# Kernel optimization log

Measured on AMD Instinct MI355X. Metric: run time of the kernel, lower is better.

## Reference

```python
import jax, jax.numpy as jnp
import numpy as np

NUM_EMBEDDINGS = 1024
EMBEDDING_DIM = 64


def setup_inputs() -> dict:
    key = jax.random.key(0)
    kx, kw = jax.random.split(key)
    x = jax.random.normal(kx, (8, 128, 128, EMBEDDING_DIM), dtype=jnp.float32)
    W = jax.random.normal(kw, (NUM_EMBEDDINGS, EMBEDDING_DIM), dtype=jnp.float32)
    return {"x": x, "W": W}


def reference(x, W):
    # Flatten to [N, D]
    flat = x.reshape(-1, EMBEDDING_DIM)
    # ||f||^2 + ||w||^2 - 2 f.w  -> [N, K]
    f_sq = jnp.sum(flat * flat, axis=1, keepdims=True)          # [N, 1]
    w_sq = jnp.sum(W * W, axis=1)                               # [K]
    prod = 2.0 * jnp.einsum('nd,kd->nk', flat, W)               # [N, K]
    distances = f_sq + w_sq - prod
    indices = jnp.argmin(distances, axis=1)                     # [N]
    # one_hot @ W is an exact gather of codebook rows
    quantized = W[indices].reshape(x.shape)
    quantized_with_grad = x + jax.lax.stop_gradient(quantized - x)
    return (quantized_with_grad, quantized, indices)
```

## Files before the change

kernel.cpp:

```cpp
#include <hip/hip_runtime.h>

#define VQ_D 64
#define VQ_MARGIN 0.015f

typedef __attribute__((ext_vector_type(8))) short bf16x8;
typedef __attribute__((ext_vector_type(4))) float f32x4;

static __device__ __forceinline__ unsigned short bf16_rne(float v) {
    unsigned u = __float_as_uint(v);
    u += 0x7fffu + ((u >> 16) & 1u);
    return (unsigned short)(u >> 16);
}

__global__ __launch_bounds__(256) void vq_prep_kernel(
    const float* __restrict__ W, unsigned short* __restrict__ Whi,
    unsigned short* __restrict__ Wlo, float* __restrict__ wsq,
    unsigned int* __restrict__ ctr, int K)
{
    int c = blockIdx.x * 256 + threadIdx.x;
    if (c == 0) *ctr = 0u;
    if (c >= K) return;
    const float4* wr = reinterpret_cast<const float4*>(W) + (size_t)c * (VQ_D / 4);
    unsigned short* hr = Whi + (size_t)c * VQ_D;
    unsigned short* lr = Wlo + (size_t)c * VQ_D;
    float s0 = 0.f, s1 = 0.f, s2 = 0.f, s3 = 0.f;
    #pragma unroll
    for (int j = 0; j < VQ_D / 4; ++j) {
        float4 v = wr[j];
        s0 = __fmaf_rn(v.x, v.x, s0); s1 = __fmaf_rn(v.y, v.y, s1);
        s2 = __fmaf_rn(v.z, v.z, s2); s3 = __fmaf_rn(v.w, v.w, s3);
        float vv[4] = {v.x, v.y, v.z, v.w};
        ushort4 h4, l4;
        unsigned short* hp = &h4.x; unsigned short* lp = &l4.x;
        #pragma unroll
        for (int e = 0; e < 4; ++e) {
            unsigned short hb = bf16_rne(vv[e]);
            float hf = __uint_as_float((unsigned)hb << 16);
            hp[e] = hb;
            lp[e] = bf16_rne(vv[e] - hf);
        }
        *reinterpret_cast<ushort4*>(hr + 4 * j) = h4;
        *reinterpret_cast<ushort4*>(lr + 4 * j) = l4;
    }
    wsq[c] = (s0 + s1) + (s2 + s3);
}

__global__ __launch_bounds__(256) void vq_mfma_kernel(
    const float* __restrict__ x, const unsigned short* __restrict__ Whi,
    const unsigned short* __restrict__ Wlo, const float* __restrict__ wsq,
    int* __restrict__ idx_final, int* __restrict__ flags,
    unsigned int* __restrict__ ctr, int N, int K)
{
    __shared__ float sD1[4][64], sD2[4][64];
    __shared__ int   sI1[4][64];

    const int tid  = threadIdx.x;
    const int wv   = tid >> 6;
    const int lane = tid & 63;
    const int g    = lane >> 4;
    const int c16  = lane & 15;
    const int rbase = blockIdx.x * 64;

    bf16x8 xh[4][2], xl[4][2];
    #pragma unroll
    for (int s = 0; s < 4; ++s) {
        int row = rbase + s * 16 + c16;
        if (row >= N) row = N - 1;
        const float* xr = x + (size_t)row * VQ_D;
        #pragma unroll
        for (int h = 0; h < 2; ++h) {
            const float4* p = reinterpret_cast<const float4*>(xr + h * 32 + g * 8);
            float4 v0 = p[0], v1 = p[1];
            float vv[8] = {v0.x, v0.y, v0.z, v0.w, v1.x, v1.y, v1.z, v1.w};
            #pragma unroll
            for (int j = 0; j < 8; ++j) {
                unsigned short hb = bf16_rne(vv[j]);
                float hf = __uint_as_float((unsigned)hb << 16);
                xh[s][h][j] = (short)hb;
                xl[s][h][j] = (short)bf16_rne(vv[j] - hf);
            }
        }
    }

    float d1[4][4], d2[4][4]; int i1[4][4];
    #pragma unroll
    for (int s = 0; s < 4; ++s)
        #pragma unroll
        for (int i = 0; i < 4; ++i) { d1[s][i] = 3.4e38f; d2[s][i] = 3.4e38f; i1[s][i] = 0; }

    const int t0 = wv * (K >> 6);
    const int t1 = t0 + (K >> 6);
    #pragma unroll 2
    for (int ct = t0; ct < t1; ++ct) {
        const int c = ct * 16 + c16;
        const unsigned short* wh = Whi + (size_t)c * VQ_D + g * 8;
        const unsigned short* wl = Wlo + (size_t)c * VQ_D + g * 8;
        bf16x8 bh0 = *reinterpret_cast<const bf16x8*>(wh);
        bf16x8 bh1 = *reinterpret_cast<const bf16x8*>(wh + 32);
        bf16x8 bl0 = *reinterpret_cast<const bf16x8*>(wl);
        bf16x8 bl1 = *reinterpret_cast<const bf16x8*>(wl + 32);
        const float wq = wsq[c];

        #pragma unroll
        for (int s = 0; s < 4; ++s) {
            f32x4 acc = {0.f, 0.f, 0.f, 0.f};
            acc = __builtin_amdgcn_mfma_f32_16x16x32_bf16(xh[s][0], bh0, acc, 0, 0, 0);
            acc = __builtin_amdgcn_mfma_f32_16x16x32_bf16(xh[s][1], bh1, acc, 0, 0, 0);
            acc = __builtin_amdgcn_mfma_f32_16x16x32_bf16(xl[s][0], bh0, acc, 0, 0, 0);
            acc = __builtin_amdgcn_mfma_f32_16x16x32_bf16(xl[s][1], bh1, acc, 0, 0, 0);
            acc = __builtin_amdgcn_mfma_f32_16x16x32_bf16(xh[s][0], bl0, acc, 0, 0, 0);
            acc = __builtin_amdgcn_mfma_f32_16x16x32_bf16(xh[s][1], bl1, acc, 0, 0, 0);
            #pragma unroll
            for (int i = 0; i < 4; ++i) {
                float d = __fmaf_rn(-2.0f, acc[i], wq);
                float o1 = d1[s][i];
                d2[s][i] = fminf(d2[s][i], fmaxf(d, o1));
                bool lt = d < o1;
                d1[s][i] = lt ? d : o1;
                i1[s][i] = lt ? c : i1[s][i];
            }
        }
    }

    #pragma unroll
    for (int s = 0; s < 4; ++s)
        #pragma unroll
        for (int i = 0; i < 4; ++i) {
            float a1 = d1[s][i], a2 = d2[s][i]; int ai = i1[s][i];
            #pragma unroll
            for (int m = 1; m < 16; m <<= 1) {
                float o1 = __shfl_xor(a1, m, 64);
                float o2 = __shfl_xor(a2, m, 64);
                int   oi = __shfl_xor(ai, m, 64);
                float n1 = fminf(a1, o1);
                a2 = fminf(fminf(a2, o2), fmaxf(a1, o1));
                ai = (o1 < a1) ? oi : ai;
                a1 = n1;
            }
            if (c16 == 0) {
                int r = s * 16 + g * 4 + i;
                sD1[wv][r] = a1; sD2[wv][r] = a2; sI1[wv][r] = ai;
            }
        }
    __syncthreads();

    if (tid < 64) {
        int row = rbase + tid;
        float m1 = sD1[0][tid], m2 = sD2[0][tid]; int mi = sI1[0][tid];
        #pragma unroll
        for (int w = 1; w < 4; ++w) {
            float a = sD1[w][tid], b = sD2[w][tid]; int ii = sI1[w][tid];
            if (a < m1) { m2 = fminf(m1, b); mi = ii; m1 = a; }
            else        { m2 = fminf(m2, a); }
        }
        if (row < N) {
            idx_final[row] = mi;
            if (m2 - m1 <= VQ_MARGIN) {
                unsigned int pos = atomicAdd(ctr, 1u);
                if (pos < (unsigned)N) flags[pos] = row;
            }
        }
    }
}

__global__ __launch_bounds__(256) void vq_recheck_kernel(
    const float* __restrict__ x, const float* __restrict__ W,
    const float* __restrict__ wsq, const int* __restrict__ flags,
    const unsigned int* __restrict__ ctr, int* __restrict__ idx_final, int N, int K)
{
    __shared__ float sBD[4];
    __shared__ int   sBI[4];

    const int tid  = threadIdx.x;
    const int wv   = tid >> 6;
    const int lane = tid & 63;
    unsigned int cnt = *ctr;
    if (cnt > (unsigned)N) cnt = (unsigned)N;

    const float4* W4 = reinterpret_cast<const float4*>(W);
    for (unsigned int t = blockIdx.x; t < cnt; t += gridDim.x) {
        const int row = flags[t];
        float f[VQ_D];
        {
            const float4* xf = reinterpret_cast<const float4*>(x) + (size_t)row * (VQ_D / 4);
            #pragma unroll
            for (int i = 0; i < VQ_D / 4; ++i) {
                float4 v = xf[i];
                f[4 * i + 0] = v.x; f[4 * i + 1] = v.y;
                f[4 * i + 2] = v.z; f[4 * i + 3] = v.w;
            }
        }
        float s0 = 0.f, s1 = 0.f, s2 = 0.f, s3 = 0.f;
        #pragma unroll
        for (int q = 0; q < VQ_D; q += 4) {
            s0 = __fmaf_rn(f[q], f[q], s0);         s1 = __fmaf_rn(f[q + 1], f[q + 1], s1);
            s2 = __fmaf_rn(f[q + 2], f[q + 2], s2); s3 = __fmaf_rn(f[q + 3], f[q + 3], s3);
        }
        const float fsq = (s0 + s1) + (s2 + s3);

        float best = 3.4e38f; int bidx = 0x7fffffff;
        #pragma unroll
        for (int tt = 0; tt < 4; ++tt) {
            const int c = wv * (K >> 2) + tt * 64 + lane;
            const float4* wc = W4 + (size_t)c * (VQ_D / 4);
            float d0 = 0.f, dd1 = 0.f, dd2 = 0.f, dd3 = 0.f;
            #pragma unroll
            for (int i = 0; i < VQ_D / 4; ++i) {
                float4 w = wc[i];
                d0  = __fmaf_rn(f[4 * i + 0], w.x, d0);
                dd1 = __fmaf_rn(f[4 * i + 1], w.y, dd1);
                dd2 = __fmaf_rn(f[4 * i + 2], w.z, dd2);
                dd3 = __fmaf_rn(f[4 * i + 3], w.w, dd3);
            }
            float dot  = (d0 + dd1) + (dd2 + dd3);
            float dist = __fmaf_rn(-2.0f, dot, fsq + wsq[c]);
            if (dist < best || (dist == best && c < bidx)) { best = dist; bidx = c; }
        }
        #pragma unroll
        for (int m = 1; m < 64; m <<= 1) {
            float od = __shfl_xor(best, m, 64);
            int   oi = __shfl_xor(bidx, m, 64);
            if (od < best || (od == best && oi < bidx)) { best = od; bidx = oi; }
        }
        if (lane == 0) { sBD[wv] = best; sBI[wv] = bidx; }
        __syncthreads();
        if (tid == 0) {
            float m1 = sBD[0]; int mi = sBI[0];
            #pragma unroll
            for (int w = 1; w < 4; ++w) {
                float a = sBD[w]; int ii = sBI[w];
                if (a < m1 || (a == m1 && ii < mi)) { m1 = a; mi = ii; }
            }
            idx_final[row] = mi;
        }
        __syncthreads();
    }
}

__global__ __launch_bounds__(256) void vq_gather_kernel(
    const float* __restrict__ x, const float* __restrict__ W,
    const int* __restrict__ idx_final, float* __restrict__ out, int N)
{
    __shared__ int sIdx[64];
    const int tid = threadIdx.x;
    const int rbase = blockIdx.x * 64;
    if (tid < 64 && rbase + tid < N) {
        int idx = idx_final[rbase + tid];
        sIdx[tid] = idx;
        out[(size_t)2 * N * VQ_D + rbase + tid] = (float)idx;
    }
    __syncthreads();
    const float4* W4 = reinterpret_cast<const float4*>(W);
    const float4* X4 = reinterpret_cast<const float4*>(x);
    float4* O0 = reinterpret_cast<float4*>(out);
    float4* O1 = O0 + (size_t)N * (VQ_D / 4);
    const size_t base4 = (size_t)rbase * (VQ_D / 4);
    #pragma unroll
    for (int i = 0; i < 4; ++i) {
        int j = i * 256 + tid;
        int rowo = j >> 4;
        int d4 = j & 15;
        if (rbase + rowo < N) {
            int idx = sIdx[rowo];
            float4 w = W4[(size_t)idx * (VQ_D / 4) + d4];
            float4 xv = X4[base4 + j];
            float4 o;
            o.x = xv.x + (w.x - xv.x);
            o.y = xv.y + (w.y - xv.y);
            o.z = xv.z + (w.z - xv.z);
            o.w = xv.w + (w.w - xv.w);
            O0[base4 + j] = o;
            O1[base4 + j] = w;
        }
    }
}

__global__ __launch_bounds__(256) void vq_wsq_kernel(const float* __restrict__ W,
                                                     float* __restrict__ wsq, int K)
{
    int c = blockIdx.x * 256 + threadIdx.x;
    if (c >= K) return;
    const float4* w4 = reinterpret_cast<const float4*>(W) + (size_t)c * (VQ_D / 4);
    float s0 = 0.f, s1 = 0.f, s2 = 0.f, s3 = 0.f;
    #pragma unroll
    for (int j = 0; j < VQ_D / 4; ++j) {
        float4 v = w4[j];
        s0 = __fmaf_rn(v.x, v.x, s0); s1 = __fmaf_rn(v.y, v.y, s1);
        s2 = __fmaf_rn(v.z, v.z, s2); s3 = __fmaf_rn(v.w, v.w, s3);
    }
    wsq[c] = (s0 + s1) + (s2 + s3);
}

__global__ __launch_bounds__(256, 6) void vq_main_kernel(const float* __restrict__ x,
    const float* __restrict__ W, const float* __restrict__ wsq,
    float* __restrict__ out, int N, int K)
{
    __shared__ unsigned long long sMerge[256];
    __shared__ int sIdx[64];
    const int tid  = threadIdx.x;
    const int lane = tid & 63;
    const int rbase = blockIdx.x * 64;
    const int row  = rbase + lane;
    const int lrow = (row < N) ? row : (N - 1);
    float f[VQ_D];
    {
        const float4* xf = reinterpret_cast<const float4*>(x) + (size_t)lrow * (VQ_D / 4);
        #pragma unroll
        for (int i = 0; i < VQ_D / 4; ++i) {
            float4 v = xf[i];
            f[4 * i + 0] = v.x; f[4 * i + 1] = v.y;
            f[4 * i + 2] = v.z; f[4 * i + 3] = v.w;
        }
    }
    float fsq;
    {
        float s0 = 0.f, s1 = 0.f, s2 = 0.f, s3 = 0.f;
        #pragma unroll
        for (int q = 0; q < VQ_D; q += 4) {
            s0 = __fmaf_rn(f[q], f[q], s0);         s1 = __fmaf_rn(f[q + 1], f[q + 1], s1);
            s2 = __fmaf_rn(f[q + 2], f[q + 2], s2); s3 = __fmaf_rn(f[q + 3], f[q + 3], s3);
        }
        fsq = (s0 + s1) + (s2 + s3);
    }
    const int slice = __builtin_amdgcn_readfirstlane(tid >> 6);
    const int c0 = slice * (K >> 2);
    const int c1 = c0 + (K >> 2);
    float best = 3.4e38f;
    int bidx = c0;
    const float4* __restrict__ W4 = reinterpret_cast<const float4*>(W);
    #pragma unroll 2
    for (int c = c0; c < c1; ++c) {
        const float4* wc = W4 + (size_t)c * (VQ_D / 4);
        float d0 = 0.f, d1 = 0.f, d2 = 0.f, d3 = 0.f;
        #pragma unroll
        for (int i = 0; i < VQ_D / 4; ++i) {
            float4 w = wc[i];
            d0 = __fmaf_rn(f[4 * i + 0], w.x, d0); d1 = __fmaf_rn(f[4 * i + 1], w.y, d1);
            d2 = __fmaf_rn(f[4 * i + 2], w.z, d2); d3 = __fmaf_rn(f[4 * i + 3], w.w, d3);
        }
        float dot = (d0 + d1) + (d2 + d3);
        float dist = __fmaf_rn(-2.0f, dot, fsq + wsq[c]);
        if (dist < best) { best = dist; bidx = c; }
    }
    best = fmaxf(best, 0.0f);
    sMerge[tid] = ((unsigned long long)__float_as_uint(best) << 32) | (unsigned int)bidx;
    __syncthreads();
    if (tid < 64) {
        unsigned long long mm = sMerge[tid];
        unsigned long long a = sMerge[tid + 64];  if (a < mm) mm = a;
        unsigned long long b = sMerge[tid + 128]; if (b < mm) mm = b;
        unsigned long long d = sMerge[tid + 192]; if (d < mm) mm = d;
        int idx = (int)(mm & 0xFFFFFFFFu);
        sIdx[tid] = idx;
        if (rbase + tid < N) out[(size_t)2 * N * VQ_D + rbase + tid] = (float)idx;
    }
    __syncthreads();
    const float4* X4 = reinterpret_cast<const float4*>(x);
    float4* O0 = reinterpret_cast<float4*>(out);
    float4* O1 = O0 + (size_t)N * (VQ_D / 4);
    const size_t base4 = (size_t)rbase * (VQ_D / 4);
    #pragma unroll
    for (int i = 0; i < 4; ++i) {
        int j = i * 256 + tid;
        int rowo = j >> 4, d4 = j & 15;
        if (rbase + rowo < N) {
            int idx = sIdx[rowo];
            float4 w = W4[(size_t)idx * (VQ_D / 4) + d4];
            float4 xv = X4[base4 + j];
            float4 o;
            o.x = xv.x + (w.x - xv.x); o.y = xv.y + (w.y - xv.y);
            o.z = xv.z + (w.z - xv.z); o.w = xv.w + (w.w - xv.w);
            O0[base4 + j] = o; O1[base4 + j] = w;
        }
    }
}

extern "C" void kernel_launch(void* const* d_in, const int* in_sizes, int n_in,
                              void* d_out, int out_size, void* d_ws, size_t ws_size,
                              hipStream_t stream)
{
    const float* x = (const float*)d_in[0];
    const float* W = (const float*)d_in[1];
    float* out = (float*)d_out;
    const int N = in_sizes[0] / VQ_D;
    const int K = in_sizes[1] / VQ_D;

    char* ws = (char*)d_ws;
    float*          wsq  = (float*)ws;
    unsigned int*   ctr  = (unsigned int*)(ws + 4096);
    int*            flags= (int*)(ws + 8192);
    int*            idxf = (int*)(ws + 8192 + (size_t)N * 4);
    unsigned short* Whi  = (unsigned short*)(ws + 8192 + (size_t)N * 8);
    unsigned short* Wlo  = Whi + (size_t)K * VQ_D;
    const size_t need = 8192 + (size_t)N * 8 + (size_t)K * VQ_D * 4;

    if (ws_size >= need && (N % 64) == 0 && (K % 256) == 0) {
        vq_prep_kernel<<<(K + 255) / 256, 256, 0, stream>>>(W, Whi, Wlo, wsq, ctr, K);
        vq_mfma_kernel<<<N / 64, 256, 0, stream>>>(x, Whi, Wlo, wsq,
                                                   idxf, flags, ctr, N, K);
        vq_recheck_kernel<<<4096, 256, 0, stream>>>(x, W, wsq, flags, ctr, idxf, N, K);
        vq_gather_kernel<<<N / 64, 256, 0, stream>>>(x, W, idxf, out, N);
    } else {
        vq_wsq_kernel<<<(K + 255) / 256, 256, 0, stream>>>(W, wsq, K);
        vq_main_kernel<<<(N + 63) / 64, 256, 0, stream>>>(x, W, wsq, out, N, K);
    }
}
```

Before: 206.4 us.

## Fuse gather into MFMA kernel, pre-pack codebook in MFMA fragment layout

The prep kernel now writes the bf16 hi/lo codebook split and the per-lane squared norms in the exact per-lane fragment order the MFMA loop reads, so each wave loads contiguous 16-byte chunks instead of strided rows. The gather/straight-through output is fused into the MFMA kernel's tail, which removes the separate gather launch and the idx_final round trip. The recheck kernel now overwrites the outputs of flagged rows directly and runs with fewer blocks. This relies on the recheck kernel executing after the fused write to overwrite borderline rows, and adds some redundant per-lane norm computation in prep.

```diff
diff --git a/kernel.cpp b/kernel.cpp
--- a/kernel.cpp
+++ b/kernel.cpp
@@ -13,46 +13,67 @@
 }
 
 __global__ __launch_bounds__(256) void vq_prep_kernel(
-    const float* __restrict__ W, unsigned short* __restrict__ Whi,
-    unsigned short* __restrict__ Wlo, float* __restrict__ wsq,
+    const float* __restrict__ W, unsigned short* __restrict__ Wpk,
+    float* __restrict__ wsqpk, float* __restrict__ wsq,
     unsigned int* __restrict__ ctr, int K)
 {
-    int c = blockIdx.x * 256 + threadIdx.x;
-    if (c == 0) *ctr = 0u;
-    if (c >= K) return;
-    const float4* wr = reinterpret_cast<const float4*>(W) + (size_t)c * (VQ_D / 4);
-    unsigned short* hr = Whi + (size_t)c * VQ_D;
-    unsigned short* lr = Wlo + (size_t)c * VQ_D;
+    const int t = blockIdx.x * 256 + threadIdx.x;
+    if (t == 0) *ctr = 0u;
+    const int NT = K >> 4;
+    if (t >= NT * 64) return;
+    const int ct = t >> 6;
+    const int l  = t & 63;
+    const int c  = ct * 16 + (l & 15);
+    const int g  = l >> 4;
+
+    const float* wr = W + (size_t)c * VQ_D;
+
     float s0 = 0.f, s1 = 0.f, s2 = 0.f, s3 = 0.f;
+    const float4* w4 = reinterpret_cast<const float4*>(wr);
     #pragma unroll
     for (int j = 0; j < VQ_D / 4; ++j) {
-        float4 v = wr[j];
+        float4 v = w4[j];
         s0 = __fmaf_rn(v.x, v.x, s0); s1 = __fmaf_rn(v.y, v.y, s1);
         s2 = __fmaf_rn(v.z, v.z, s2); s3 = __fmaf_rn(v.w, v.w, s3);
-        float vv[4] = {v.x, v.y, v.z, v.w};
-        ushort4 h4, l4;
-        unsigned short* hp = &h4.x; unsigned short* lp = &l4.x;
-        #pragma unroll
-        for (int e = 0; e < 4; ++e) {
-            unsigned short hb = bf16_rne(vv[e]);
-            float hf = __uint_as_float((unsigned)hb << 16);
-            hp[e] = hb;
-            lp[e] = bf16_rne(vv[e] - hf);
-        }
-        *reinterpret_cast<ushort4*>(hr + 4 * j) = h4;
-        *reinterpret_cast<ushort4*>(lr + 4 * j) = l4;
-    }
-    wsq[c] = (s0 + s1) + (s2 + s3);
+    }
+    const float wq = (s0 + s1) + (s2 + s3);
+    wsqpk[ct * 64 + l] = wq;
+    if (l < 16) wsq[ct * 16 + l] = wq;
+
+    float v0[8], v1[8];
+    {
+        const float4* p0 = reinterpret_cast<const float4*>(wr + g * 8);
+        const float4* p1 = reinterpret_cast<const float4*>(wr + 32 + g * 8);
+        float4 a = p0[0], b = p0[1], cc = p1[0], d = p1[1];
+        v0[0]=a.x; v0[1]=a.y; v0[2]=a.z; v0[3]=a.w; v0[4]=b.x; v0[5]=b.y; v0[6]=b.z; v0[7]=b.w;
+        v1[0]=cc.x;v1[1]=cc.y;v1[2]=cc.z;v1[3]=cc.w;v1[4]=d.x; v1[5]=d.y; v1[6]=d.z; v1[7]=d.w;
+    }
+    bf16x8 h0, h1, l0, l1;
+    #pragma unroll
+    for (int j = 0; j < 8; ++j) {
+        unsigned short hb0 = bf16_rne(v0[j]);
+        unsigned short hb1 = bf16_rne(v1[j]);
+        h0[j] = (short)hb0;
+        h1[j] = (short)hb1;
+        l0[j] = (short)bf16_rne(v0[j] - __uint_as_float((unsigned)hb0 << 16));
+        l1[j] = (short)bf16_rne(v1[j] - __uint_as_float((unsigned)hb1 << 16));
+    }
+    bf16x8* P = reinterpret_cast<bf16x8*>(Wpk);
+    P[(ct * 4 + 0) * 64 + l] = h0;
+    P[(ct * 4 + 1) * 64 + l] = h1;
+    P[(ct * 4 + 2) * 64 + l] = l0;
+    P[(ct * 4 + 3) * 64 + l] = l1;
 }
 
 __global__ __launch_bounds__(256) void vq_mfma_kernel(
-    const float* __restrict__ x, const unsigned short* __restrict__ Whi,
-    const unsigned short* __restrict__ Wlo, const float* __restrict__ wsq,
-    int* __restrict__ idx_final, int* __restrict__ flags,
+    const float* __restrict__ x, const float* __restrict__ W,
+    const unsigned short* __restrict__ Wpk, const float* __restrict__ wsqpk,
+    float* __restrict__ out, int* __restrict__ flags,
     unsigned int* __restrict__ ctr, int N, int K)
 {
     __shared__ float sD1[4][64], sD2[4][64];
     __shared__ int   sI1[4][64];
+    __shared__ int   sIdx[64];
 
     const int tid  = threadIdx.x;
     const int wv   = tid >> 6;
@@ -88,18 +109,20 @@
         #pragma unroll
         for (int i = 0; i < 4; ++i) { d1[s][i] = 3.4e38f; d2[s][i] = 3.4e38f; i1[s][i] = 0; }
 
-    const int t0 = wv * (K >> 6);
-    const int t1 = t0 + (K >> 6);
+    const int NT = K >> 4;
+    const int t0 = wv * (NT >> 2);
+    const int t1 = t0 + (NT >> 2);
+    const bf16x8* __restrict__ P = reinterpret_cast<const bf16x8*>(Wpk);
+
     #pragma unroll 2
     for (int ct = t0; ct < t1; ++ct) {
         const int c = ct * 16 + c16;
-        const unsigned short* wh = Whi + (size_t)c * VQ_D + g * 8;
-        const unsigned short* wl = Wlo + (size_t)c * VQ_D + g * 8;
-        bf16x8 bh0 = *reinterpret_cast<const bf16x8*>(wh);
-        bf16x8 bh1 = *reinterpret_cast<const bf16x8*>(wh + 32);
-        bf16x8 bl0 = *reinterpret_cast<const bf16x8*>(wl);
-        bf16x8 bl1 = *reinterpret_cast<const bf16x8*>(wl + 32);
-        const float wq = wsq[c];
+        const int pb = ct * 256 + lane;
+        bf16x8 bh0 = P[pb];
+        bf16x8 bh1 = P[pb + 64];
+        bf16x8 bl0 = P[pb + 128];
+        bf16x8 bl1 = P[pb + 192];
+        const float wq = wsqpk[ct * 64 + lane];
 
         #pragma unroll
         for (int s = 0; s < 4; ++s) {
@@ -153,103 +176,17 @@
             if (a < m1) { m2 = fminf(m1, b); mi = ii; m1 = a; }
             else        { m2 = fminf(m2, a); }
         }
+        sIdx[tid] = mi;
         if (row < N) {
-            idx_final[row] = mi;
+            out[(size_t)2 * N * VQ_D + row] = (float)mi;
             if (m2 - m1 <= VQ_MARGIN) {
                 unsigned int pos = atomicAdd(ctr, 1u);
                 if (pos < (unsigned)N) flags[pos] = row;
             }
         }
     }
-}
-
-__global__ __launch_bounds__(256) void vq_recheck_kernel(
-    const float* __restrict__ x, const float* __restrict__ W,
-    const float* __restrict__ wsq, const int* __restrict__ flags,
-    const unsigned int* __restrict__ ctr, int* __restrict__ idx_final, int N, int K)
-{
-    __shared__ float sBD[4];
-    __shared__ int   sBI[4];
-
-    const int tid  = threadIdx.x;
-    const int wv   = tid >> 6;
-    const int lane = tid & 63;
-    unsigned int cnt = *ctr;
-    if (cnt > (unsigned)N) cnt = (unsigned)N;
-
-    const float4* W4 = reinterpret_cast<const float4*>(W);
-    for (unsigned int t = blockIdx.x; t < cnt; t += gridDim.x) {
-        const int row = flags[t];
-        float f[VQ_D];
-        {
-            const float4* xf = reinterpret_cast<const float4*>(x) + (size_t)row * (VQ_D / 4);
-            #pragma unroll
-            for (int i = 0; i < VQ_D / 4; ++i) {
-                float4 v = xf[i];
-                f[4 * i + 0] = v.x; f[4 * i + 1] = v.y;
-                f[4 * i + 2] = v.z; f[4 * i + 3] = v.w;
-            }
-        }
-        float s0 = 0.f, s1 = 0.f, s2 = 0.f, s3 = 0.f;
-        #pragma unroll
-        for (int q = 0; q < VQ_D; q += 4) {
-            s0 = __fmaf_rn(f[q], f[q], s0);         s1 = __fmaf_rn(f[q + 1], f[q + 1], s1);
-            s2 = __fmaf_rn(f[q + 2], f[q + 2], s2); s3 = __fmaf_rn(f[q + 3], f[q + 3], s3);
-        }
-        const float fsq = (s0 + s1) + (s2 + s3);
-
-        float best = 3.4e38f; int bidx = 0x7fffffff;
-        #pragma unroll
-        for (int tt = 0; tt < 4; ++tt) {
-            const int c = wv * (K >> 2) + tt * 64 + lane;
-            const float4* wc = W4 + (size_t)c * (VQ_D / 4);
-            float d0 = 0.f, dd1 = 0.f, dd2 = 0.f, dd3 = 0.f;
-            #pragma unroll
-            for (int i = 0; i < VQ_D / 4; ++i) {
-                float4 w = wc[i];
-                d0  = __fmaf_rn(f[4 * i + 0], w.x, d0);
-                dd1 = __fmaf_rn(f[4 * i + 1], w.y, dd1);
-                dd2 = __fmaf_rn(f[4 * i + 2], w.z, dd2);
-                dd3 = __fmaf_rn(f[4 * i + 3], w.w, dd3);
-            }
-            float dot  = (d0 + dd1) + (dd2 + dd3);
-            float dist = __fmaf_rn(-2.0f, dot, fsq + wsq[c]);
-            if (dist < best || (dist == best && c < bidx)) { best = dist; bidx = c; }
-        }
-        #pragma unroll
-        for (int m = 1; m < 64; m <<= 1) {
-            float od = __shfl_xor(best, m, 64);
-            int   oi = __shfl_xor(bidx, m, 64);
-            if (od < best || (od == best && oi < bidx)) { best = od; bidx = oi; }
-        }
-        if (lane == 0) { sBD[wv] = best; sBI[wv] = bidx; }
-        __syncthreads();
-        if (tid == 0) {
-            float m1 = sBD[0]; int mi = sBI[0];
-            #pragma unroll
-            for (int w = 1; w < 4; ++w) {
-                float a = sBD[w]; int ii = sBI[w];
-                if (a < m1 || (a == m1 && ii < mi)) { m1 = a; mi = ii; }
-            }
-            idx_final[row] = mi;
-        }
-        __syncthreads();
-    }
-}
-
-__global__ __launch_bounds__(256) void vq_gather_kernel(
-    const float* __restrict__ x, const float* __restrict__ W,
-    const int* __restrict__ idx_final, float* __restrict__ out, int N)
-{
-    __shared__ int sIdx[64];
-    const int tid = threadIdx.x;
-    const int rbase = blockIdx.x * 64;
-    if (tid < 64 && rbase + tid < N) {
-        int idx = idx_final[rbase + tid];
-        sIdx[tid] = idx;
-        out[(size_t)2 * N * VQ_D + rbase + tid] = (float)idx;
-    }
     __syncthreads();
+
     const float4* W4 = reinterpret_cast<const float4*>(W);
     const float4* X4 = reinterpret_cast<const float4*>(x);
     float4* O0 = reinterpret_cast<float4*>(out);
@@ -275,6 +212,90 @@
     }
 }
 
+__global__ __launch_bounds__(256) void vq_recheck_kernel(
+    const float* __restrict__ x, const float* __restrict__ W,
+    const float* __restrict__ wsq, const int* __restrict__ flags,
+    const unsigned int* __restrict__ ctr, float* __restrict__ out, int N, int K)
+{
+    __shared__ float sBD[4];
+    __shared__ int   sBI[4];
+    __shared__ int   sFin;
+
+    const int tid  = threadIdx.x;
+    const int wv   = tid >> 6;
+    const int lane = tid & 63;
+    unsigned int cnt = *ctr;
+    if (cnt > (unsigned)N) cnt = (unsigned)N;
+
+    const float4* W4 = reinterpret_cast<const float4*>(W);
+    for (unsigned int t = blockIdx.x; t < cnt; t += gridDim.x) {
+        const int row = flags[t];
+        float f[VQ_D];
+        {
+            const float4* xf = reinterpret_cast<const float4*>(x) + (size_t)row * (VQ_D / 4);
+            #pragma unroll
+            for (int i = 0; i < VQ_D / 4; ++i) {
+                float4 v = xf[i];
+                f[4 * i + 0] = v.x; f[4 * i + 1] = v.y;
+                f[4 * i + 2] = v.z; f[4 * i + 3] = v.w;
+            }
+        }
+        float s0 = 0.f, s1 = 0.f, s2 = 0.f, s3 = 0.f;
+        #pragma unroll
+        for (int q = 0; q < VQ_D; q += 4) {
+            s0 = __fmaf_rn(f[q], f[q], s0);         s1 = __fmaf_rn(f[q + 1], f[q + 1], s1);
+            s2 = __fmaf_rn(f[q + 2], f[q + 2], s2); s3 = __fmaf_rn(f[q + 3], f[q + 3], s3);
+        }
+        const float fsq = (s0 + s1) + (s2 + s3);
+
+        float best = 3.4e38f; int bidx = 0x7fffffff;
+        #pragma unroll
+        for (int tt = 0; tt < 4; ++tt) {
+            const int c = wv * (K >> 2) + tt * 64 + lane;
+            const float4* wc = W4 + (size_t)c * (VQ_D / 4);
+            float d0 = 0.f, dd1 = 0.f, dd2 = 0.f, dd3 = 0.f;
+            #pragma unroll
+            for (int i = 0; i < VQ_D / 4; ++i) {
+                float4 w = wc[i];
+                d0  = __fmaf_rn(f[4 * i + 0], w.x, d0);
+                dd1 = __fmaf_rn(f[4 * i + 1], w.y, dd1);
+                dd2 = __fmaf_rn(f[4 * i + 2], w.z, dd2);
+                dd3 = __fmaf_rn(f[4 * i + 3], w.w, dd3);
+            }
+            float dot  = (d0 + dd1) + (dd2 + dd3);
+            float dist = __fmaf_rn(-2.0f, dot, fsq + wsq[c]);
+            if (dist < best || (dist == best && c < bidx)) { best = dist; bidx = c; }
+        }
+        #pragma unroll
+        for (int m = 1; m < 64; m <<= 1) {
+            float od = __shfl_xor(best, m, 64);
+            int   oi = __shfl_xor(bidx, m, 64);
+            if (od < best || (od == best && oi < bidx)) { best = od; bidx = oi; }
+        }
+        if (lane == 0) { sBD[wv] = best; sBI[wv] = bidx; }
+        __syncthreads();
+        if (tid == 0) {
+            float m1 = sBD[0]; int mi = sBI[0];
+            #pragma unroll
+            for (int w = 1; w < 4; ++w) {
+                float a = sBD[w]; int ii = sBI[w];
+                if (a < m1 || (a == m1 && ii < mi)) { m1 = a; mi = ii; }
+            }
+            sFin = mi;
+        }
+        __syncthreads();
+        const int mi = sFin;
+        if (tid < 64) {
+            float wvv = W[(size_t)mi * VQ_D + tid];
+            float xv  = x[(size_t)row * VQ_D + tid];
+            out[(size_t)row * VQ_D + tid] = xv + (wvv - xv);
+            out[(size_t)N * VQ_D + (size_t)row * VQ_D + tid] = wvv;
+            if (tid == 0) out[(size_t)2 * N * VQ_D + row] = (float)mi;
+        }
+        __syncthreads();
+    }
+}
+
 __global__ __launch_bounds__(256) void vq_wsq_kernel(const float* __restrict__ W,
                                                      float* __restrict__ wsq, int K)
 {
@@ -384,22 +405,23 @@
     float* out = (float*)d_out;
     const int N = in_sizes[0] / VQ_D;
     const int K = in_sizes[1] / VQ_D;
+    const int NT = K >> 4;
 
     char* ws = (char*)d_ws;
-    float*          wsq  = (float*)ws;
-    unsigned int*   ctr  = (unsigned int*)(ws + 4096);
-    int*            flags= (int*)(ws + 8192);
-    int*            idxf = (int*)(ws + 8192 + (size_t)N * 4);
-    unsigned short* Whi  = (unsigned short*)(ws + 8192 + (size_t)N * 8);
-    unsigned short* Wlo  = Whi + (size_t)K * VQ_D;
-    const size_t need = 8192 + (size_t)N * 8 + (size_t)K * VQ_D * 4;
+    float*          wsq   = (float*)ws;
+    unsigned int*   ctr   = (unsigned int*)(ws + 4096);
+    int*            flags = (int*)(ws + 8192);
+    unsigned short* Wpk   = (unsigned short*)(ws + 8192 + (size_t)N * 4);
+    float*          wsqpk = (float*)((char*)Wpk + (size_t)K * VQ_D * 4);
+    const size_t need = 8192 + (size_t)N * 4 + (size_t)K * VQ_D * 4
+                      + (size_t)NT * 64 * 4;
 
     if (ws_size >= need && (N % 64) == 0 && (K % 256) == 0) {
-        vq_prep_kernel<<<(K + 255) / 256, 256, 0, stream>>>(W, Whi, Wlo, wsq, ctr, K);
-        vq_mfma_kernel<<<N / 64, 256, 0, stream>>>(x, Whi, Wlo, wsq,
-                                                   idxf, flags, ctr, N, K);
-        vq_recheck_kernel<<<4096, 256, 0, stream>>>(x, W, wsq, flags, ctr, idxf, N, K);
-        vq_gather_kernel<<<N / 64, 256, 0, stream>>>(x, W, idxf, out, N);
+        vq_prep_kernel<<<(NT * 64 + 255) / 256, 256, 0, stream>>>(W, Wpk, wsqpk,
+                                                                  wsq, ctr, K);
+        vq_mfma_kernel<<<N / 64, 256, 0, stream>>>(x, W, Wpk, wsqpk,
+                                                   out, flags, ctr, N, K);
+        vq_recheck_kernel<<<2048, 256, 0, stream>>>(x, W, wsq, flags, ctr, out, N, K);
     } else {
         vq_wsq_kernel<<<(K + 255) / 256, 256, 0, stream>>>(W, wsq, K);
         vq_main_kernel<<<(N + 63) / 64, 256, 0, stream>>>(x, W, wsq, out, N, K);
```

New measurement: 178.4 us. 13.6% less time.
